# Performance work log

Measured on AMD Instinct MI355X. Metric: run time of the kernel, lower is better.

Reference implementation:

```python
import jax, jax.numpy as jnp
import numpy as np
import math

B, D_MODEL, H, D_K, L = 24, 128, 8, 16, 512


def setup_inputs() -> dict:
    key = jax.random.key(0)
    ks = jax.random.split(key, 5)
    x = jax.random.normal(ks[0], (B, D_MODEL, L), dtype=jnp.float32)
    Wq = jax.random.normal(ks[1], (H, B, D_K, D_MODEL), dtype=jnp.float32)
    Wk = jax.random.normal(ks[2], (H, B, D_K, D_MODEL), dtype=jnp.float32)
    Wv = jax.random.normal(ks[3], (H, B, D_K, D_MODEL), dtype=jnp.float32)
    Wo = jax.random.normal(ks[4], (B, H * D_K, D_MODEL), dtype=jnp.float32)
    return {"x": x, "Wq": Wq, "Wk": Wk, "Wv": Wv, "Wo": Wo}


def reference(x, Wq, Wk, Wv, Wo):
    # Per-head, per-batch projections: [h,b,k,d] @ [b,d,l] -> [h,b,k,l]
    Q = jnp.einsum('hbkd,bdl->hbkl', Wq, x)
    K = jnp.einsum('hbkd,bdl->hbkl', Wk, x)
    V = jnp.einsum('hbkd,bdl->hbkl', Wv, x)
    # scores[h,b,l,m] = Q[:, :, :, l] . K[:, :, :, m]; torch softmax dim=1 of
    # the [B, L, L] score -> softmax over the QUERY axis l (axis=2 here).
    scores = jnp.einsum('hbkl,hbkm->hblm', Q, K) / math.sqrt(D_K)
    attn = jax.nn.softmax(scores, axis=2)
    # head_i = V @ attn : [h,b,v,l] @ [h,b,l,m] -> [h,b,v,m]
    heads = jnp.einsum('hbvl,hblm->hbvm', V, attn)
    # concat heads along channel dim: [b, h*v, L]
    head = heads.transpose(1, 0, 2, 3).reshape(B, H * D_K, L)
    # out = Wo @ head : [b, h*v, d_model] treated as [b,128,128] @ [b,128,L]
    out = jnp.einsum('bod,bdl->bol', Wo, head)
    return out
```

## Files before the change

kernel.cpp:

```cpp
#include <hip/hip_runtime.h>
#include <math.h>

#define NB 24
#define DM 128
#define NH 8
#define DK 16
#define LL 512
#define HB (NH * NB)

#define QB_OFF   0
#define KB_OFF   6291456
#define VB_OFF   12582912
#define HEAD_OFF 15728640

typedef __attribute__((ext_vector_type(8))) short bf16x8;
typedef __attribute__((ext_vector_type(4))) float f32x4;
typedef __attribute__((ext_vector_type(4))) int   i32x4;

#define MFMA  __builtin_amdgcn_mfma_f32_16x16x32_bf16
#define EXP2  __builtin_amdgcn_exp2f
#define BPERM __builtin_amdgcn_ds_bpermute

static __device__ __forceinline__ unsigned bfr(float x) {
    return (__float_as_uint(x) + 0x8000u) & 0xffff0000u;
}
static __device__ __forceinline__ unsigned pk2(unsigned e, unsigned o) {
    return (e >> 16) | o;
}

static __device__ __forceinline__ void store_split_row(
    unsigned short* __restrict__ row, const float* a, float scale)
{
    unsigned hi[16], lo[16];
    #pragma unroll
    for (int k = 0; k < 16; ++k) {
        const float v = a[k] * scale;
        hi[k] = bfr(v);
        lo[k] = bfr(v - __uint_as_float(hi[k]));
    }
    uint4* r = (uint4*)row;
    uint4 d0 = { pk2(hi[0],hi[1]),  pk2(hi[2],hi[3]),  pk2(hi[4],hi[5]),  pk2(hi[6],hi[7]) };
    uint4 d1 = { pk2(hi[8],hi[9]),  pk2(hi[10],hi[11]),pk2(hi[12],hi[13]),pk2(hi[14],hi[15]) };
    uint4 d2 = { pk2(lo[0],lo[1]),  pk2(lo[2],lo[3]),  pk2(lo[4],lo[5]),  pk2(lo[6],lo[7]) };
    uint4 d3 = { pk2(lo[8],lo[9]),  pk2(lo[10],lo[11]),pk2(lo[12],lo[13]),pk2(lo[14],lo[15]) };
    r[0] = d0; r[1] = d1; r[2] = d2; r[3] = d3;
}

__global__ __launch_bounds__(256)
void qkv_proj(const float* __restrict__ x,
              const float* __restrict__ Wq,
              const float* __restrict__ Wk,
              const float* __restrict__ Wv,
              unsigned short* __restrict__ qb,
              unsigned short* __restrict__ kb,
              unsigned short* __restrict__ vb)
{
    const int blk = blockIdx.x;
    const int hb  = blk / 3;
    const int mat = blk - hb * 3;
    const int l0  = threadIdx.x;
    const int l1  = threadIdx.x + 256;
    const int b   = hb % NB;

    const float* __restrict__ xb = x + (size_t)b * DM * LL;
    const float* __restrict__ W =
        (mat == 0 ? Wq : (mat == 1 ? Wk : Wv)) + (size_t)hb * DK * DM;

    float a0[DK], a1[DK];
    #pragma unroll
    for (int k = 0; k < DK; ++k) { a0[k] = 0.f; a1[k] = 0.f; }

    #pragma unroll 4
    for (int d = 0; d < DM; ++d) {
        const float x0 = xb[(size_t)d * LL + l0];
        const float x1 = xb[(size_t)d * LL + l1];
        #pragma unroll
        for (int k = 0; k < DK; ++k) {
            const float w = W[k * DM + d];
            a0[k] = fmaf(w, x0, a0[k]);
            a1[k] = fmaf(w, x1, a1[k]);
        }
    }

    if (mat == 2) {
        unsigned short* __restrict__ vo = vb + (size_t)hb * DK * LL;
        #pragma unroll
        for (int k = 0; k < DK; ++k) {
            vo[(size_t)k * LL + l0] = (unsigned short)(bfr(a0[k]) >> 16);
            vo[(size_t)k * LL + l1] = (unsigned short)(bfr(a1[k]) >> 16);
        }
    } else {
        const float scale = (mat == 1) ? (0.25f * 1.44269504f) : 1.0f;
        unsigned short* __restrict__ base =
            (mat == 0 ? qb : kb) + (size_t)hb * LL * 32;
        store_split_row(base + (size_t)l0 * 32, a0, scale);
        store_split_row(base + (size_t)l1 * 32, a1, scale);
    }
}

static __device__ __forceinline__ void soft_pv(
    const f32x4& s0, const f32x4& s1, float tm, float& bar, float& sm,
    f32x4& O, const bf16x8& aV, int aLo, int aHi, bool up)
{
    const float nb = fmaxf(bar, tm + 32.f);
    const float f  = EXP2(bar - nb);
    bar = nb;
    const unsigned u0 = bfr(EXP2(s0[0]-nb)), u1 = bfr(EXP2(s0[1]-nb));
    const unsigned u2 = bfr(EXP2(s0[2]-nb)), u3 = bfr(EXP2(s0[3]-nb));
    const unsigned w0 = bfr(EXP2(s1[0]-nb)), w1 = bfr(EXP2(s1[1]-nb));
    const unsigned w2 = bfr(EXP2(s1[2]-nb)), w3 = bfr(EXP2(s1[3]-nb));
    const float sacc =
        ((__uint_as_float(u0) + __uint_as_float(u1)) +
         (__uint_as_float(u2) + __uint_as_float(u3))) +
        ((__uint_as_float(w0) + __uint_as_float(w1)) +
         (__uint_as_float(w2) + __uint_as_float(w3)));
    sm = fmaf(sm, f, sacc);
    O *= f;
    const int c0 = (int)pk2(u0, u1), c1 = (int)pk2(u2, u3);
    const int c2 = (int)pk2(w0, w1), c3 = (int)pk2(w2, w3);
    const int p00 = BPERM(aLo, c0), p02 = BPERM(aLo, c2);
    const int p10 = BPERM(aLo, c1), p12 = BPERM(aLo, c3);
    const int p20 = BPERM(aHi, c0), p22 = BPERM(aHi, c2);
    const int p30 = BPERM(aHi, c1), p32 = BPERM(aHi, c3);
    i32x4 bi = { up ? p00 : p02, up ? p10 : p12,
                 up ? p20 : p22, up ? p30 : p32 };
    O = MFMA(aV, __builtin_bit_cast(bf16x8, bi), O, 0, 0, 0);
}

__global__ __launch_bounds__(256)
void attn_mfma(const unsigned short* __restrict__ qb,
               const unsigned short* __restrict__ kb,
               const unsigned short* __restrict__ vb,
               float* __restrict__ head)
{
    const int hb   = blockIdx.x >> 2;
    const int mc   = blockIdx.x & 3;
    const int tid  = threadIdx.x;
    const int wave = tid >> 6;
    const int lane = tid & 63;
    const int g    = lane >> 4;
    const int mR   = lane & 15;
    const int mb   = mc * 128 + wave * 32;

    const unsigned short* Kr0 = kb + ((size_t)hb * LL + mb + mR) * 32;
    const unsigned short* Kr1 = Kr0 + 16 * 32;
    const bf16x8 bK0  = *(const bf16x8*)(Kr0 + g * 8);
    const bf16x8 bK0s = *(const bf16x8*)(Kr0 + (g ^ 2) * 8);
    const bf16x8 bK1  = *(const bf16x8*)(Kr1 + g * 8);
    const bf16x8 bK1s = *(const bf16x8*)(Kr1 + (g ^ 2) * 8);

    const unsigned short* qrow =
        qb + ((size_t)hb * LL + mR) * 32 + g * 8;
    const unsigned short* vrow = vb + ((size_t)hb * DK + mR) * LL + g * 8;

    f32x4 O0 = {0.f,0.f,0.f,0.f}, O1 = {0.f,0.f,0.f,0.f};
    float bar0 = -1e30f, bar1 = -1e30f, sm0 = 0.f, sm1 = 0.f;

    const int aLo = ((g & 1) * 32 + mR) * 4;
    const int aHi = aLo + 64;
    const bool up = (g < 2);

    for (int l = 0; l < LL; l += 32) {
        const bf16x8 aQ0 = *(const bf16x8*)(qrow + (size_t)l * 32);
        const bf16x8 aQ1 = *(const bf16x8*)(qrow + (size_t)(l + 16) * 32);

        const f32x4 z = {0.f,0.f,0.f,0.f};
        f32x4 sA0 = MFMA(aQ0, bK0, z, 0,0,0);  sA0 = MFMA(aQ0, bK0s, sA0, 0,0,0);
        f32x4 sB0 = MFMA(aQ0, bK1, z, 0,0,0);  sB0 = MFMA(aQ0, bK1s, sB0, 0,0,0);
        f32x4 sA1 = MFMA(aQ1, bK0, z, 0,0,0);  sA1 = MFMA(aQ1, bK0s, sA1, 0,0,0);
        f32x4 sB1 = MFMA(aQ1, bK1, z, 0,0,0);  sB1 = MFMA(aQ1, bK1s, sB1, 0,0,0);

        float tmA = fmaxf(fmaxf(fmaxf(sA0[0],sA0[1]), fmaxf(sA0[2],sA0[3])),
                          fmaxf(fmaxf(sA1[0],sA1[1]), fmaxf(sA1[2],sA1[3])));
        float tmB = fmaxf(fmaxf(fmaxf(sB0[0],sB0[1]), fmaxf(sB0[2],sB0[3])),
                          fmaxf(fmaxf(sB1[0],sB1[1]), fmaxf(sB1[2],sB1[3])));
        tmA = fmaxf(tmA, __shfl_xor(tmA, 16, 64));
        tmA = fmaxf(tmA, __shfl_xor(tmA, 32, 64));
        tmB = fmaxf(tmB, __shfl_xor(tmB, 16, 64));
        tmB = fmaxf(tmB, __shfl_xor(tmB, 32, 64));

        if (__any(tmA + 64.f > bar0) || __any(tmB + 64.f > bar1)) {
            const bf16x8 aV = *(const bf16x8*)(vrow + l);
            soft_pv(sA0, sA1, tmA, bar0, sm0, O0, aV, aLo, aHi, up);
            soft_pv(sB0, sB1, tmB, bar1, sm1, O1, aV, aLo, aHi, up);
        }
    }

    sm0 += __shfl_xor(sm0, 16, 64);  sm0 += __shfl_xor(sm0, 32, 64);
    sm1 += __shfl_xor(sm1, 16, 64);  sm1 += __shfl_xor(sm1, 32, 64);
    const float i0 = 1.f / sm0, i1 = 1.f / sm1;

    const int h = hb / NB, bb = hb % NB;
    float* __restrict__ ho =
        head + (size_t)(bb * DM + h * DK + 4 * g) * LL + mb + mR;
    #pragma unroll
    for (int i = 0; i < 4; ++i) {
        ho[(size_t)i * LL]      = O0[i] * i0;
        ho[(size_t)i * LL + 16] = O1[i] * i1;
    }
}

__global__ __launch_bounds__(256)
void out_proj(const float* __restrict__ Wo,
              const float* __restrict__ head,
              float* __restrict__ out)
{
    const int blk  = blockIdx.x;
    const int b    = blk >> 5;
    const int rc   = (blk >> 1) & 15;
    const int cc   = blk & 1;
    const int col  = cc * 256 + threadIdx.x;
    const int row0 = rc * 8;

    const float* __restrict__ wo = Wo + (size_t)b * DM * DM + (size_t)row0 * DM;
    const float* __restrict__ hd = head + (size_t)b * DM * LL + col;

    float acc[8];
    #pragma unroll
    for (int i = 0; i < 8; ++i) acc[i] = 0.f;

    #pragma unroll 4
    for (int d = 0; d < DM; ++d) {
        const float hv = hd[(size_t)d * LL];
        #pragma unroll
        for (int i = 0; i < 8; ++i)
            acc[i] = fmaf(wo[i * DM + d], hv, acc[i]);
    }

    float* __restrict__ ob = out + (size_t)b * DM * LL + (size_t)row0 * LL + col;
    #pragma unroll
    for (int i = 0; i < 8; ++i)
        ob[(size_t)i * LL] = acc[i];
}

extern "C" void kernel_launch(void* const* d_in, const int* in_sizes, int n_in,
                              void* d_out, int out_size, void* d_ws, size_t ws_size,
                              hipStream_t stream) {
    const float* x  = (const float*)d_in[0];
    const float* Wq = (const float*)d_in[1];
    const float* Wk = (const float*)d_in[2];
    const float* Wv = (const float*)d_in[3];
    const float* Wo = (const float*)d_in[4];
    float* out = (float*)d_out;

    char* ws = (char*)d_ws;
    unsigned short* qb   = (unsigned short*)(ws + QB_OFF);
    unsigned short* kb   = (unsigned short*)(ws + KB_OFF);
    unsigned short* vb   = (unsigned short*)(ws + VB_OFF);
    float*          head = (float*)(ws + HEAD_OFF);

    qkv_proj <<<HB * 3, 256, 0, stream>>>(x, Wq, Wk, Wv, qb, kb, vb);
    attn_mfma<<<HB * 4, 256, 0, stream>>>(qb, kb, vb, head);
    out_proj <<<NB * 32, 256, 0, stream>>>(Wo, head, out);
}
```

Baseline: 133.3 us.

## Move QKV and output projections onto bf16 MFMA with a split-precision prep pass

A new prep kernel transposes x and splits it and the QKV weights into bf16 hi/lo pairs, and converts Wo to bf16. The QKV projection then runs on MFMA using three products per tile (hi*hi, hi*lo, lo*hi), and the output projection runs on single-bf16 MFMA. Attention now writes the head tensor as transposed bf16 rather than fp32. This replaces the scalar fp32 FMA projection loops with matrix-core work and halves the size of the head tensor. In exchange it adds a fourth launch plus extra workspace traffic, and the bf16-only output projection and head tensor lower precision.

```diff
diff --git a/kernel.cpp b/kernel.cpp
--- a/kernel.cpp
+++ b/kernel.cpp
@@ -8,10 +8,15 @@
 #define LL 512
 #define HB (NH * NB)
 
-#define QB_OFF   0
-#define KB_OFF   6291456
-#define VB_OFF   12582912
-#define HEAD_OFF 15728640
+#define XTH_OFF 0
+#define XTL_OFF 3145728
+#define WHI_OFF 6291456
+#define WLO_OFF 8650752
+#define WOB_OFF 11010048
+#define QB_OFF  11796480
+#define KB_OFF  18087936
+#define VB_OFF  24379392
+#define HT_OFF  27525120
 
 typedef __attribute__((ext_vector_type(8))) short bf16x8;
 typedef __attribute__((ext_vector_type(4))) float f32x4;
@@ -28,73 +33,134 @@
     return (e >> 16) | o;
 }
 
-static __device__ __forceinline__ void store_split_row(
-    unsigned short* __restrict__ row, const float* a, float scale)
-{
-    unsigned hi[16], lo[16];
-    #pragma unroll
-    for (int k = 0; k < 16; ++k) {
-        const float v = a[k] * scale;
-        hi[k] = bfr(v);
-        lo[k] = bfr(v - __uint_as_float(hi[k]));
-    }
-    uint4* r = (uint4*)row;
-    uint4 d0 = { pk2(hi[0],hi[1]),  pk2(hi[2],hi[3]),  pk2(hi[4],hi[5]),  pk2(hi[6],hi[7]) };
-    uint4 d1 = { pk2(hi[8],hi[9]),  pk2(hi[10],hi[11]),pk2(hi[12],hi[13]),pk2(hi[14],hi[15]) };
-    uint4 d2 = { pk2(lo[0],lo[1]),  pk2(lo[2],lo[3]),  pk2(lo[4],lo[5]),  pk2(lo[6],lo[7]) };
-    uint4 d3 = { pk2(lo[8],lo[9]),  pk2(lo[10],lo[11]),pk2(lo[12],lo[13]),pk2(lo[14],lo[15]) };
-    r[0] = d0; r[1] = d1; r[2] = d2; r[3] = d3;
-}
-
 __global__ __launch_bounds__(256)
-void qkv_proj(const float* __restrict__ x,
-              const float* __restrict__ Wq,
-              const float* __restrict__ Wk,
-              const float* __restrict__ Wv,
+void prep(const float* __restrict__ x,
+          const float* __restrict__ Wq,
+          const float* __restrict__ Wk,
+          const float* __restrict__ Wv,
+          const float* __restrict__ Wo,
+          unsigned short* __restrict__ xthi,
+          unsigned short* __restrict__ xtlo,
+          unsigned short* __restrict__ whi,
+          unsigned short* __restrict__ wlo,
+          unsigned short* __restrict__ wob)
+{
+    __shared__ float T[128][65];
+    const int bid = blockIdx.x, tid = threadIdx.x;
+
+    if (bid < 192) {
+        const int b = bid >> 3, lc = bid & 7;
+        const float* __restrict__ xb = x + (size_t)b * 65536 + lc * 64;
+        #pragma unroll
+        for (int i = 0; i < 32; ++i) {
+            const int idx = i * 256 + tid;
+            T[idx >> 6][idx & 63] = xb[(size_t)(idx >> 6) * LL + (idx & 63)];
+        }
+        __syncthreads();
+        #pragma unroll
+        for (int i = 0; i < 32; ++i) {
+            const int idx = i * 256 + tid;
+            const int l = idx >> 7, d = idx & 127;
+            const float v = T[d][l];
+            const unsigned h = bfr(v);
+            const size_t o = (size_t)b * 65536 + (size_t)(lc * 64 + l) * DM + d;
+            xthi[o] = (unsigned short)(h >> 16);
+            xtlo[o] = (unsigned short)(bfr(v - __uint_as_float(h)) >> 16);
+        }
+    } else if (bid < 768) {
+        const int w = bid - 192, hb = w / 3, mat = w - hb * 3;
+        const float* __restrict__ src =
+            (mat == 0 ? Wq : (mat == 1 ? Wk : Wv)) + (size_t)hb * 2048;
+        unsigned short* __restrict__ dh = whi + (size_t)w * 2048;
+        unsigned short* __restrict__ dl = wlo + (size_t)w * 2048;
+        for (int i = tid; i < 2048; i += 256) {
+            const float v = src[i];
+            const unsigned h = bfr(v);
+            dh[i] = (unsigned short)(h >> 16);
+            dl[i] = (unsigned short)(bfr(v - __uint_as_float(h)) >> 16);
+        }
+    } else {
+        const int w = bid - 768;
+        const float* __restrict__ src = Wo + (size_t)w * 4096;
+        unsigned short* __restrict__ d = wob + (size_t)w * 4096;
+        for (int i = tid; i < 4096; i += 256)
+            d[i] = (unsigned short)(bfr(src[i]) >> 16);
+    }
+}
+
+__global__ __launch_bounds__(256)
+void qkv_mfma(const unsigned short* __restrict__ xthi,
+              const unsigned short* __restrict__ xtlo,
+              const unsigned short* __restrict__ whi,
+              const unsigned short* __restrict__ wlo,
               unsigned short* __restrict__ qb,
               unsigned short* __restrict__ kb,
               unsigned short* __restrict__ vb)
 {
-    const int blk = blockIdx.x;
-    const int hb  = blk / 3;
-    const int mat = blk - hb * 3;
-    const int l0  = threadIdx.x;
-    const int l1  = threadIdx.x + 256;
-    const int b   = hb % NB;
-
-    const float* __restrict__ xb = x + (size_t)b * DM * LL;
-    const float* __restrict__ W =
-        (mat == 0 ? Wq : (mat == 1 ? Wk : Wv)) + (size_t)hb * DK * DM;
-
-    float a0[DK], a1[DK];
-    #pragma unroll
-    for (int k = 0; k < DK; ++k) { a0[k] = 0.f; a1[k] = 0.f; }
-
-    #pragma unroll 4
-    for (int d = 0; d < DM; ++d) {
-        const float x0 = xb[(size_t)d * LL + l0];
-        const float x1 = xb[(size_t)d * LL + l1];
-        #pragma unroll
-        for (int k = 0; k < DK; ++k) {
-            const float w = W[k * DM + d];
-            a0[k] = fmaf(w, x0, a0[k]);
-            a1[k] = fmaf(w, x1, a1[k]);
+    const int blk  = blockIdx.x;
+    const int nc   = blk & 1;
+    const int hm   = blk >> 1;
+    const int mat  = hm % 3;
+    const int hb   = hm / 3;
+    const int b    = hb % NB;
+    const int wv   = threadIdx.x >> 6;
+    const int lane = threadIdx.x & 63;
+    const int g = lane >> 4, mR = lane & 15;
+    const int l0 = nc * 256 + wv * 64;
+
+    const unsigned short* __restrict__ wA = whi + (size_t)hm * 2048 + mR * 128 + g * 8;
+    const unsigned short* __restrict__ wB = wlo + (size_t)hm * 2048 + mR * 128 + g * 8;
+    const unsigned short* __restrict__ xh = xthi + (size_t)b * 65536 + g * 8;
+    const unsigned short* __restrict__ xl = xtlo + (size_t)b * 65536 + g * 8;
+
+    f32x4 C[4];
+    #pragma unroll
+    for (int t = 0; t < 4; ++t) C[t] = (f32x4){0.f, 0.f, 0.f, 0.f};
+
+    #pragma unroll
+    for (int kk = 0; kk < 4; ++kk) {
+        const bf16x8 aH = *(const bf16x8*)(wA + kk * 32);
+        const bf16x8 aL = *(const bf16x8*)(wB + kk * 32);
+        #pragma unroll
+        for (int t = 0; t < 4; ++t) {
+            const size_t lo_ = (size_t)(l0 + t * 16 + mR) * DM + kk * 32;
+            const bf16x8 bH = *(const bf16x8*)(xh + lo_);
+            const bf16x8 bL = *(const bf16x8*)(xl + lo_);
+            C[t] = MFMA(aH, bH, C[t], 0, 0, 0);
+            C[t] = MFMA(aH, bL, C[t], 0, 0, 0);
+            C[t] = MFMA(aL, bH, C[t], 0, 0, 0);
         }
     }
 
     if (mat == 2) {
-        unsigned short* __restrict__ vo = vb + (size_t)hb * DK * LL;
-        #pragma unroll
-        for (int k = 0; k < DK; ++k) {
-            vo[(size_t)k * LL + l0] = (unsigned short)(bfr(a0[k]) >> 16);
-            vo[(size_t)k * LL + l1] = (unsigned short)(bfr(a1[k]) >> 16);
+        unsigned short* __restrict__ vo = vb + (size_t)hb * 8192;
+        #pragma unroll
+        for (int t = 0; t < 4; ++t) {
+            const int l = l0 + t * 16 + mR;
+            #pragma unroll
+            for (int i = 0; i < 4; ++i)
+                vo[(size_t)(4 * g + i) * LL + l] =
+                    (unsigned short)(bfr(C[t][i]) >> 16);
         }
     } else {
         const float scale = (mat == 1) ? (0.25f * 1.44269504f) : 1.0f;
-        unsigned short* __restrict__ base =
+        unsigned short* __restrict__ dst =
             (mat == 0 ? qb : kb) + (size_t)hb * LL * 32;
-        store_split_row(base + (size_t)l0 * 32, a0, scale);
-        store_split_row(base + (size_t)l1 * 32, a1, scale);
+        #pragma unroll
+        for (int t = 0; t < 4; ++t) {
+            const int l = l0 + t * 16 + mR;
+            ushort4 hi4, lo4;
+            #pragma unroll
+            for (int i = 0; i < 4; ++i) {
+                const float v = C[t][i] * scale;
+                const unsigned h = bfr(v);
+                const unsigned lw = bfr(v - __uint_as_float(h));
+                ((unsigned short*)&hi4)[i] = (unsigned short)(h >> 16);
+                ((unsigned short*)&lo4)[i] = (unsigned short)(lw >> 16);
+            }
+            *(ushort4*)(dst + (size_t)l * 32 + 4 * g)      = hi4;
+            *(ushort4*)(dst + (size_t)l * 32 + 16 + 4 * g) = lo4;
+        }
     }
 }
 
@@ -131,7 +197,7 @@
 void attn_mfma(const unsigned short* __restrict__ qb,
                const unsigned short* __restrict__ kb,
                const unsigned short* __restrict__ vb,
-               float* __restrict__ head)
+               unsigned short* __restrict__ ht)
 {
     const int hb   = blockIdx.x >> 2;
     const int mc   = blockIdx.x & 3;
@@ -149,8 +215,7 @@
     const bf16x8 bK1  = *(const bf16x8*)(Kr1 + g * 8);
     const bf16x8 bK1s = *(const bf16x8*)(Kr1 + (g ^ 2) * 8);
 
-    const unsigned short* qrow =
-        qb + ((size_t)hb * LL + mR) * 32 + g * 8;
+    const unsigned short* qrow = qb + ((size_t)hb * LL + mR) * 32 + g * 8;
     const unsigned short* vrow = vb + ((size_t)hb * DK + mR) * LL + g * 8;
 
     f32x4 O0 = {0.f,0.f,0.f,0.f}, O1 = {0.f,0.f,0.f,0.f};
@@ -191,46 +256,53 @@
     const float i0 = 1.f / sm0, i1 = 1.f / sm1;
 
     const int h = hb / NB, bb = hb % NB;
-    float* __restrict__ ho =
-        head + (size_t)(bb * DM + h * DK + 4 * g) * LL + mb + mR;
+    unsigned short* __restrict__ ho =
+        ht + (size_t)bb * 65536 + (size_t)(mb + mR) * DM + h * 16 + 4 * g;
+    ushort4 p0, p1;
     #pragma unroll
     for (int i = 0; i < 4; ++i) {
-        ho[(size_t)i * LL]      = O0[i] * i0;
-        ho[(size_t)i * LL + 16] = O1[i] * i1;
-    }
+        ((unsigned short*)&p0)[i] = (unsigned short)(bfr(O0[i] * i0) >> 16);
+        ((unsigned short*)&p1)[i] = (unsigned short)(bfr(O1[i] * i1) >> 16);
+    }
+    *(ushort4*)ho              = p0;
+    *(ushort4*)(ho + 16 * DM)  = p1;
 }
 
 __global__ __launch_bounds__(256)
-void out_proj(const float* __restrict__ Wo,
-              const float* __restrict__ head,
+void out_mfma(const unsigned short* __restrict__ wob,
+              const unsigned short* __restrict__ ht,
               float* __restrict__ out)
 {
     const int blk  = blockIdx.x;
     const int b    = blk >> 5;
-    const int rc   = (blk >> 1) & 15;
-    const int cc   = blk & 1;
-    const int col  = cc * 256 + threadIdx.x;
-    const int row0 = rc * 8;
-
-    const float* __restrict__ wo = Wo + (size_t)b * DM * DM + (size_t)row0 * DM;
-    const float* __restrict__ hd = head + (size_t)b * DM * LL + col;
-
-    float acc[8];
-    #pragma unroll
-    for (int i = 0; i < 8; ++i) acc[i] = 0.f;
-
-    #pragma unroll 4
-    for (int d = 0; d < DM; ++d) {
-        const float hv = hd[(size_t)d * LL];
-        #pragma unroll
-        for (int i = 0; i < 8; ++i)
-            acc[i] = fmaf(wo[i * DM + d], hv, acc[i]);
-    }
-
-    float* __restrict__ ob = out + (size_t)b * DM * LL + (size_t)row0 * LL + col;
-    #pragma unroll
-    for (int i = 0; i < 8; ++i)
-        ob[(size_t)i * LL] = acc[i];
+    const int mq   = (blk >> 4) & 1;
+    const int nq   = blk & 15;
+    const int wv   = threadIdx.x >> 6;
+    const int lane = threadIdx.x & 63;
+    const int g = lane >> 4, mR = lane & 15;
+    const int m0 = (mq * 4 + wv) * 16;
+    const int n0 = nq * 32;
+
+    const unsigned short* __restrict__ A =
+        wob + (size_t)b * 16384 + (size_t)(m0 + mR) * DM + g * 8;
+    const unsigned short* __restrict__ B = ht + (size_t)b * 65536 + g * 8;
+
+    f32x4 C0 = {0.f,0.f,0.f,0.f}, C1 = {0.f,0.f,0.f,0.f};
+    #pragma unroll
+    for (int kk = 0; kk < 4; ++kk) {
+        const bf16x8 aW = *(const bf16x8*)(A + kk * 32);
+        const bf16x8 b0 = *(const bf16x8*)(B + (size_t)(n0 + mR) * DM + kk * 32);
+        const bf16x8 b1 = *(const bf16x8*)(B + (size_t)(n0 + 16 + mR) * DM + kk * 32);
+        C0 = MFMA(aW, b0, C0, 0, 0, 0);
+        C1 = MFMA(aW, b1, C1, 0, 0, 0);
+    }
+
+    float* __restrict__ ob = out + (size_t)b * 65536 + (size_t)(m0 + 4 * g) * LL;
+    #pragma unroll
+    for (int i = 0; i < 4; ++i) {
+        ob[(size_t)i * LL + n0 + mR]      = C0[i];
+        ob[(size_t)i * LL + n0 + 16 + mR] = C1[i];
+    }
 }
 
 extern "C" void kernel_launch(void* const* d_in, const int* in_sizes, int n_in,
@@ -244,12 +316,18 @@
     float* out = (float*)d_out;
 
     char* ws = (char*)d_ws;
+    unsigned short* xthi = (unsigned short*)(ws + XTH_OFF);
+    unsigned short* xtlo = (unsigned short*)(ws + XTL_OFF);
+    unsigned short* whi  = (unsigned short*)(ws + WHI_OFF);
+    unsigned short* wlo  = (unsigned short*)(ws + WLO_OFF);
+    unsigned short* wob  = (unsigned short*)(ws + WOB_OFF);
     unsigned short* qb   = (unsigned short*)(ws + QB_OFF);
     unsigned short* kb   = (unsigned short*)(ws + KB_OFF);
     unsigned short* vb   = (unsigned short*)(ws + VB_OFF);
-    float*          head = (float*)(ws + HEAD_OFF);
-
-    qkv_proj <<<HB * 3, 256, 0, stream>>>(x, Wq, Wk, Wv, qb, kb, vb);
-    attn_mfma<<<HB * 4, 256, 0, stream>>>(qb, kb, vb, head);
-    out_proj <<<NB * 32, 256, 0, stream>>>(Wo, head, out);
-}
+    unsigned short* ht   = (unsigned short*)(ws + HT_OFF);
+
+    prep     <<<864,     256, 0, stream>>>(x, Wq, Wk, Wv, Wo, xthi, xtlo, whi, wlo, wob);
+    qkv_mfma <<<HB * 6,  256, 0, stream>>>(xthi, xtlo, whi, wlo, qb, kb, vb);
+    attn_mfma<<<HB * 4,  256, 0, stream>>>(qb, kb, vb, ht);
+    out_mfma <<<NB * 32, 256, 0, stream>>>(wob, ht, out);
+}
```

Measured after the change: 126.9 us. 1.05x faster.
